# Kernel optimization log

Measured on AMD Instinct MI355X. Metric: run time of the kernel, lower is better.

The kernel has to match this reference:

```python
import jax, jax.numpy as jnp
import numpy as np
import math

DIM = 32
CODEBOOK_SIZE = 16384
LOG_N = int(math.log(CODEBOOK_SIZE, 2))  # 14
LOGVAR_MIN, LOGVAR_MAX = -30.0, 20.0
TOL = 0.5
BETA = 1.0
LAM = 1.0
LAM_MIN = 1.0
LAM_MAX = 1.0
HALF_LOG_2PI = 0.5 * math.log(2.0 * math.pi)


def setup_inputs() -> dict:
    key = jax.random.key(0)
    k1, k2, k3 = jax.random.split(key, 3)
    z = jax.random.normal(k1, (4, 512, 512), dtype=jnp.float32)
    noise = jax.random.normal(k2, (2048, 256), dtype=jnp.float32)
    # prior_samples buffer: standard-normal codebook [K, DIM]
    codebook = jax.random.normal(k3, (CODEBOOK_SIZE, DIM), dtype=jnp.float32)
    return {"z": z, "noise": noise, "codebook": codebook}


def _forward(z, noise, codebook):
    z_shape = z.shape
    zf = z.reshape(-1, z_shape[-1])                       # [N_tok, 2*DIM*cb]
    cb_num = zf.shape[-1] // (2 * DIM)                    # codebook_num
    mu, logvar = jnp.split(zf, 2, axis=-1)                # each [N_tok, DIM*cb]
    logvar = jnp.clip(logvar, LOGVAR_MIN, LOGVAR_MAX)
    std = jnp.exp(0.5 * logvar)
    var = jnp.exp(logvar)

    # ---- quant_gaussian ----
    zhat_g = mu + noise * std                             # reparam sample
    kl2 = 1.4426 * 0.5 * (mu * mu + var - 1.0 - logvar)
    kl2 = kl2.reshape(-1, DIM, cb_num).sum(axis=1)        # [N_tok, cb]
    ge = (kl2 > LOG_N + TOL).astype(kl2.dtype) * LAM_MAX
    eq = ((kl2 <= LOG_N + TOL) & (kl2 >= LOG_N - TOL)).astype(kl2.dtype)
    le = (kl2 < LOG_N - TOL).astype(kl2.dtype) * LAM_MIN
    kl_loss = jnp.mean(ge * kl2 + eq * kl2 + le * kl2) * LAM

    # ---- quant_vq (Gaussian log-likelihood-ratio codebook search) ----
    # rows: (token, codebook_num) pairs, each with a DIM-dim Gaussian
    mu_r = mu.reshape(-1, DIM, cb_num).transpose(0, 2, 1).reshape(-1, DIM)    # [N, DIM]
    std_r = std.reshape(-1, DIM, cb_num).transpose(0, 2, 1).reshape(-1, DIM)  # [N, DIM]
    inv_var = 1.0 / (std_r * std_r)                                           # [N, DIM]

    c = codebook                                          # [K, DIM]
    c2 = c * c
    # sum_d Normal(mu, std).log_prob(c) expanded into GEMMs over DIM:
    #   -sum log std - DIM/2*log(2pi) - 0.5*(c^2 - 2 c mu + mu^2) / var
    termA = -jnp.sum(jnp.log(std_r), axis=-1) - DIM * HALF_LOG_2PI            # [N]
    quad = 0.5 * (jnp.einsum('nd,kd->nk', inv_var, c2)
                  - 2.0 * jnp.einsum('nd,kd->nk', mu_r * inv_var, c)
                  + jnp.sum(mu_r * mu_r * inv_var, axis=-1, keepdims=True))   # [N, K]
    prior_lp = jnp.sum(-0.5 * c2 - HALF_LOG_2PI, axis=-1)                     # [K]
    perturbed = termA[:, None] - quad - BETA * prior_lp[None, :]              # [N, K]

    indices = jnp.argmax(perturbed, axis=1)               # [N]
    zhat_v = c[indices]                                   # [N, DIM]

    zhat_v = zhat_v.reshape(-1, cb_num, DIM).transpose(0, 2, 1).reshape(-1, cb_num * DIM)
    zhat_v = zhat_v.reshape(*z_shape[:-1], -1)            # [..., DIM*cb]
    zhat_g = zhat_g.reshape(*z_shape[:-1], -1)
    indices = indices.reshape(*z_shape[:-1], cb_num)

    # straight-through estimator (use_ste=True); vq branch is no_grad in torch
    zhat = zhat_g - jax.lax.stop_gradient(zhat_g) + jax.lax.stop_gradient(zhat_v)
    return zhat, kl_loss, indices


def reference(z, noise, codebook):
    return _forward(z, noise, codebook)
```

## Files before the change

kernel.cpp:

```cpp
#include <hip/hip_runtime.h>
#include <math.h>


typedef _Float16 half8 __attribute__((ext_vector_type(8)));
typedef float f32x4 __attribute__((ext_vector_type(4)));

#define DIM 32
#define NROWS 16384
#define NSPLIT 16
#define SPLITK 1024
#define NCOL 256

#define WS_M1   0
#define WS_KL   256
#define WS_PQ   4096
#define WS_AH   (WS_PQ + 4194304)
#define WS_BH   (WS_AH + 2097152)
#define WS_W1   (WS_BH + 2097152)

__global__ __launch_bounds__(256) void prep_kernel(const float* __restrict__ cb,
                                                   const float* __restrict__ z,
                                                   _Float16* __restrict__ Bh,
                                                   float* __restrict__ M1,
                                                   float* __restrict__ PQ,
                                                   _Float16* __restrict__ Ah,
                                                   double* __restrict__ klsum) {
  const int w = threadIdx.x >> 6, l = threadIdx.x & 63;
  const int sub = l >> 5, d = l & 31;
  if (blockIdx.x < 512) {
    __shared__ float lm[8][DIM];
    float m = 0.0f;
#pragma unroll
    for (int i = 0; i < 4; ++i) {
      const int k = blockIdx.x * 32 + i * 8 + w * 2 + sub;
      const float c = cb[k * DIM + d];
      const int key = k & 7;
      const int sc = (d >> 3) ^ key;
      const int sq = (4 + (d >> 3)) ^ key;
      Bh[(size_t)k * 64 + sc * 8 + (d & 7)] = (_Float16)c;
      Bh[(size_t)k * 64 + sq * 8 + (d & 7)] = (_Float16)(c * c);
      m = fmaxf(m, fabsf(c));
    }
    lm[threadIdx.x >> 5][d] = m;
    __syncthreads();
    if (threadIdx.x < DIM) {
      float x = lm[0][threadIdx.x];
#pragma unroll
      for (int i = 1; i < 8; ++i) x = fmaxf(x, lm[i][threadIdx.x]);
      atomicMax((unsigned*)&M1[threadIdx.x], __float_as_uint(x));
    }
  } else {
    const int blk = blockIdx.x - 512;
    double kacc = 0.0;
#pragma unroll 1
    for (int i = 0; i < 4; ++i) {
      const int row = blk * 32 + i * 8 + w * 2 + sub;
      const int t = row >> 3, c = row & 7;
      const float mu = z[t * 512 + d * 8 + c];
      float lv = z[t * 512 + 256 + d * 8 + c];
      lv = fminf(fmaxf(lv, -30.0f), 20.0f);
      const float stdv = expf(0.5f * lv);
      const float iv = 1.0f / (stdv * stdv);
      const float p = mu * iv;
      const float q = 0.5f * (1.0f - iv);
      PQ[(size_t)row * 64 + d] = p;
      PQ[(size_t)row * 64 + 32 + d] = q;
      Ah[(size_t)row * 64 + d] = (_Float16)p;
      Ah[(size_t)row * 64 + 32 + d] = (_Float16)q;
      kacc += (double)(mu * mu + stdv * stdv - 1.0f - lv);
    }
#pragma unroll
    for (int off = 32; off > 0; off >>= 1) kacc += __shfl_down(kacc, off);
    __shared__ double wsum[4];
    if (l == 0) wsum[w] = kacc;
    __syncthreads();
    if (threadIdx.x == 0)
      atomicAdd(klsum, (wsum[0] + wsum[1]) + (wsum[2] + wsum[3]));
  }
}

__device__ __forceinline__ void gload_lds16(const _Float16* g, _Float16* l) {
  __builtin_amdgcn_global_load_lds(
      (__attribute__((address_space(1))) void*)(g),
      (__attribute__((address_space(3))) void*)(l), 16, 0, 0);
}

__global__ __launch_bounds__(256, 4) void filter_kernel(const _Float16* __restrict__ Ah,
                                                        const _Float16* __restrict__ Bh,
                                                        float* __restrict__ W1) {
  __shared__ _Float16 sB[2][8192];
  const int tid = threadIdx.x;
  const int lane = tid & 63;
  const int wave = tid >> 6;
  const int split = blockIdx.y;
  const int rowbase = blockIdx.x * 256 + wave * 64;
  const int c16 = lane & 15, quad = lane >> 4;

  const _Float16* gB = Bh + (size_t)split * SPLITK * 64;

#pragma unroll
  for (int j = 0; j < 4; ++j)
    gload_lds16(gB + j * 2048 + tid * 8, &sB[0][j * 2048 + tid * 8]);

  half8 uh0[4], uh1[4];
#pragma unroll
  for (int rt = 0; rt < 4; ++rt) {
    const size_t abase = (size_t)(rowbase + rt * 16 + c16) * 64 + quad * 8;
    uh0[rt] = *(const half8*)(Ah + abase);
    uh1[rt] = *(const half8*)(Ah + abase + 32);
  }

  float a1[4][4];
#pragma unroll
  for (int rt = 0; rt < 4; ++rt)
#pragma unroll
    for (int r = 0; r < 4; ++r) a1[rt][r] = -INFINITY;

  const f32x4 fzero = {0.f, 0.f, 0.f, 0.f};
  const int key = c16 & 7;
  const int rs0h = c16 * 64 + (quad ^ key) * 8;
  const int rs1h = c16 * 64 + ((quad + 4) ^ key) * 8;

  __syncthreads();

#pragma unroll 1
  for (int ch = 0; ch < 8; ++ch) {
    if (ch < 7) {
      const _Float16* src = gB + (size_t)(ch + 1) * 8192;
      _Float16* dst = &sB[(ch + 1) & 1][0];
#pragma unroll
      for (int j = 0; j < 4; ++j)
        gload_lds16(src + j * 2048 + tid * 8, dst + j * 2048 + tid * 8);
    }
    const _Float16* buf = &sB[ch & 1][0];
#pragma unroll 1
    for (int tp = 0; tp < 4; ++tp) {
      const _Float16* b0 = buf + (2 * tp) * 1024;
      const _Float16* b1 = b0 + 1024;
      const half8 x0 = *(const half8*)(b0 + rs0h);
      const half8 x1 = *(const half8*)(b0 + rs1h);
      const half8 y0 = *(const half8*)(b1 + rs0h);
      const half8 y1 = *(const half8*)(b1 + rs1h);
#pragma unroll
      for (int rt = 0; rt < 4; ++rt) {
        f32x4 h0 = __builtin_amdgcn_mfma_f32_16x16x32_f16(uh0[rt], x0, fzero, 0, 0, 0);
        h0 = __builtin_amdgcn_mfma_f32_16x16x32_f16(uh1[rt], x1, h0, 0, 0, 0);
        f32x4 h1 = __builtin_amdgcn_mfma_f32_16x16x32_f16(uh0[rt], y0, fzero, 0, 0, 0);
        h1 = __builtin_amdgcn_mfma_f32_16x16x32_f16(uh1[rt], y1, h1, 0, 0, 0);
#pragma unroll
        for (int r = 0; r < 4; ++r)
          a1[rt][r] = fmaxf(fmaxf(h0[r], h1[r]), a1[rt][r]);
      }
    }
    __syncthreads();
  }

#pragma unroll
  for (int rt = 0; rt < 4; ++rt)
#pragma unroll
    for (int r = 0; r < 4; ++r) {
      const int row_r = rowbase + rt * 16 + quad * 4 + r;
      W1[((size_t)split * NROWS + row_r) * 16 + c16] = a1[rt][r];
    }
}

__device__ __forceinline__ float exact_score(const float4* __restrict__ cb4,
                                             const float4* __restrict__ spq,
                                             int k) {
  float s0 = 0.0f, s1 = 0.0f, s2 = 0.0f, s3 = 0.0f;
#pragma unroll
  for (int m = 0; m < 8; ++m) {
    const float4 cv = cb4[k * 8 + m];
    const float4 pv = spq[m];
    const float4 qv = spq[8 + m];
    s0 = fmaf(cv.x, fmaf(qv.x, cv.x, pv.x), s0);
    s1 = fmaf(cv.y, fmaf(qv.y, cv.y, pv.y), s1);
    s2 = fmaf(cv.z, fmaf(qv.z, cv.z, pv.z), s2);
    s3 = fmaf(cv.w, fmaf(qv.w, cv.w, pv.w), s3);
  }
  return (s0 + s1) + (s2 + s3);
}

__global__ __launch_bounds__(256, 4) void merge_kernel(const float* __restrict__ PQ,
                                                       const float* __restrict__ cb,
                                                       const float* __restrict__ W1,
                                                       const float* __restrict__ M1,
                                                       const double* __restrict__ klsum,
                                                       float* __restrict__ out0,
                                                       float* __restrict__ out1,
                                                       float* __restrict__ out2) {
  __shared__ float4 spq_s[4][16];
  const int lane = threadIdx.x & 63;
  const int wave = threadIdx.x >> 6;
  const int row = blockIdx.x * 4 + wave;

  if (lane < 16)
    spq_s[wave][lane] = ((const float4*)(PQ + (size_t)row * 64))[lane];
  __syncthreads();
  const float4* spq = spq_s[wave];
  const float4* __restrict__ cb4 = (const float4*)cb;

  float s = 0.0f;
  if (lane < DIM) {
    const float m1 = M1[lane];
    const float pd = ((const float*)spq)[lane];
    const float qd = ((const float*)spq)[32 + lane];
    s = fabsf(pd) * m1 + fabsf(qd) * m1 * m1;
  }
#pragma unroll
  for (int off = 1; off < 32; off <<= 1) s += __shfl_xor(s, off);
  const float Sn = __shfl(s, 0);

  float w[4];
#pragma unroll
  for (int i = 0; i < 4; ++i)
    w[i] = W1[((size_t)(i * 4 + (lane >> 4)) * NROWS + row) * 16 + (lane & 15)];
  float As = fmaxf(fmaxf(w[0], w[1]), fmaxf(w[2], w[3]));
#pragma unroll
  for (int off = 1; off < 64; off <<= 1) As = fmaxf(As, __shfl_xor(As, off));
  const float Btot = 1.05e-3f * Sn + 2e-5f * (fabsf(As) + 1.0f) + 1e-3f;

  int done_col = -1;
#pragma unroll
  for (int i = 0; i < 4; ++i) {
    if (done_col < 0) {
      const unsigned long long m = __ballot(w[i] == As);
      if (m) done_col = i * 64 + __builtin_ctzll(m);
    }
  }
  const int k0 = (done_col >> 4) * SPLITK + lane * 16 + (done_col & 15);
  float best = exact_score(cb4, spq, k0);
  int bk = k0;
#pragma unroll
  for (int off = 1; off < 64; off <<= 1) {
    const float ov = __shfl_xor(best, off);
    const int ok = __shfl_xor(bk, off);
    if (ov > best || (ov == best && ok < bk)) { best = ov; bk = ok; }
  }
  const float Estar = best;

#pragma unroll 1
  for (int i = 0; i < 4; ++i) {
    unsigned long long m = __ballot(w[i] + Btot >= Estar);
    if ((done_col >> 6) == i) m &= ~(1ull << (done_col & 63));
    while (m) {
      const int e = __builtin_ctzll(m);
      m &= m - 1;
      const int col = i * 64 + e;
      const int k = (col >> 4) * SPLITK + lane * 16 + (col & 15);
      const float sc = exact_score(cb4, spq, k);
      if (sc > best || (sc == best && k < bk)) { best = sc; bk = k; }
    }
  }
#pragma unroll
  for (int off = 1; off < 64; off <<= 1) {
    const float ov = __shfl_xor(best, off);
    const int ok = __shfl_xor(bk, off);
    if (ov > best || (ov == best && ok < bk)) { best = ov; bk = ok; }
  }
  if (lane == 0) out2[row] = (float)bk;
  const int tt = row >> 3, cc = row & 7;
  if (lane < DIM) out0[tt * 256 + lane * 8 + cc] = cb[bk * DIM + lane];
  if (blockIdx.x == 0 && threadIdx.x == 0)
    out1[0] = (float)(klsum[0] * (1.4426 * 0.5) / (double)NROWS);
}

extern "C" void kernel_launch(void* const* d_in, const int* in_sizes, int n_in,
                              void* d_out, int out_size, void* d_ws, size_t ws_size,
                              hipStream_t stream) {
  const float* z  = (const float*)d_in[0];
  const float* cb = (const float*)d_in[2];

  char* ws = (char*)d_ws;
  float*      M1 = (float*)(ws + WS_M1);
  double* klsum  = (double*)(ws + WS_KL);
  float*      PQ = (float*)(ws + WS_PQ);
  _Float16*   Ah = (_Float16*)(ws + WS_AH);
  _Float16*   Bh = (_Float16*)(ws + WS_BH);
  float*      W1 = (float*)(ws + WS_W1);

  float* out0 = (float*)d_out;
  float* out1 = out0 + 524288;
  float* out2 = out1 + 1;

  (void)hipMemsetAsync(ws, 0, 4096, stream);
  prep_kernel<<<1024, 256, 0, stream>>>(cb, z, Bh, M1, PQ, Ah, klsum);
  dim3 fgrid(64, NSPLIT);
  filter_kernel<<<fgrid, 256, 0, stream>>>(Ah, Bh, W1);
  merge_kernel<<<NROWS / 4, 256, 0, stream>>>(PQ, cb, W1, M1, klsum,
                                              out0, out1, out2);
}
```

Measured before the change: 134.8 us.

## Keep codebook tiles in registers and stream rows through MFMA filter

The filter kernel is restructured so each block holds a 128-entry codebook slice in registers and streams 512 query rows per wave from global memory. This drops the LDS double-buffering and the block barriers. Partial maxima now cover contiguous groups of 64 codebook entries, reduced across lanes with shuffles, and W1 is stored column-major so the merge kernel can read it coalesced. The merge kernel also swizzles its block order. In exchange there are more cross-lane shuffles and scattered per-row stores, and codebook grouping changes, which alters which candidates get rescored.

```diff
diff --git a/kernel.cpp b/kernel.cpp
--- a/kernel.cpp
+++ b/kernel.cpp
@@ -7,8 +7,11 @@
 
 #define DIM 32
 #define NROWS 16384
-#define NSPLIT 16
-#define SPLITK 1024
+#define KSIZE 16384
+#define KBLK 128
+#define NKB (KSIZE / KBLK)
+#define RGRP 8
+#define NRT 32
 #define NCOL 256
 
 #define WS_M1   0
@@ -34,11 +37,8 @@
     for (int i = 0; i < 4; ++i) {
       const int k = blockIdx.x * 32 + i * 8 + w * 2 + sub;
       const float c = cb[k * DIM + d];
-      const int key = k & 7;
-      const int sc = (d >> 3) ^ key;
-      const int sq = (4 + (d >> 3)) ^ key;
-      Bh[(size_t)k * 64 + sc * 8 + (d & 7)] = (_Float16)c;
-      Bh[(size_t)k * 64 + sq * 8 + (d & 7)] = (_Float16)(c * c);
+      Bh[(size_t)k * 64 + d] = (_Float16)c;
+      Bh[(size_t)k * 64 + 32 + d] = (_Float16)(c * c);
       m = fmaxf(m, fabsf(c));
     }
     lm[threadIdx.x >> 5][d] = m;
@@ -79,89 +79,73 @@
   }
 }
 
-__device__ __forceinline__ void gload_lds16(const _Float16* g, _Float16* l) {
-  __builtin_amdgcn_global_load_lds(
-      (__attribute__((address_space(1))) void*)(g),
-      (__attribute__((address_space(3))) void*)(l), 16, 0, 0);
-}
-
 __global__ __launch_bounds__(256, 4) void filter_kernel(const _Float16* __restrict__ Ah,
                                                         const _Float16* __restrict__ Bh,
                                                         float* __restrict__ W1) {
-  __shared__ _Float16 sB[2][8192];
-  const int tid = threadIdx.x;
-  const int lane = tid & 63;
-  const int wave = tid >> 6;
-  const int split = blockIdx.y;
-  const int rowbase = blockIdx.x * 256 + wave * 64;
+  const int lane = threadIdx.x & 63;
+  const int wave = threadIdx.x >> 6;
   const int c16 = lane & 15, quad = lane >> 4;
-
-  const _Float16* gB = Bh + (size_t)split * SPLITK * 64;
-
-#pragma unroll
-  for (int j = 0; j < 4; ++j)
-    gload_lds16(gB + j * 2048 + tid * 8, &sB[0][j * 2048 + tid * 8]);
-
-  half8 uh0[4], uh1[4];
-#pragma unroll
-  for (int rt = 0; rt < 4; ++rt) {
-    const size_t abase = (size_t)(rowbase + rt * 16 + c16) * 64 + quad * 8;
-    uh0[rt] = *(const half8*)(Ah + abase);
-    uh1[rt] = *(const half8*)(Ah + abase + 32);
-  }
-
-  float a1[4][4];
-#pragma unroll
-  for (int rt = 0; rt < 4; ++rt)
-#pragma unroll
-    for (int r = 0; r < 4; ++r) a1[rt][r] = -INFINITY;
+  const int kbase = blockIdx.y * KBLK;
+  const int col0 = blockIdx.y * 2;
+  const int rowbase0 = blockIdx.x * 2048 + wave * 512;
+
+  half8 bx0[8], bx1[8];
+#pragma unroll
+  for (int t = 0; t < 8; ++t) {
+    const size_t bb = (size_t)(kbase + t * 16 + c16) * 64 + quad * 8;
+    bx0[t] = *(const half8*)(Bh + bb);
+    bx1[t] = *(const half8*)(Bh + bb + 32);
+  }
 
   const f32x4 fzero = {0.f, 0.f, 0.f, 0.f};
-  const int key = c16 & 7;
-  const int rs0h = c16 * 64 + (quad ^ key) * 8;
-  const int rs1h = c16 * 64 + ((quad + 4) ^ key) * 8;
-
-  __syncthreads();
+  const size_t astep = 16 * 64;
+  size_t acur = (size_t)(rowbase0 + c16) * 64 + quad * 8;
+  half8 u0 = *(const half8*)(Ah + acur);
+  half8 u1 = *(const half8*)(Ah + acur + 32);
 
 #pragma unroll 1
-  for (int ch = 0; ch < 8; ++ch) {
-    if (ch < 7) {
-      const _Float16* src = gB + (size_t)(ch + 1) * 8192;
-      _Float16* dst = &sB[(ch + 1) & 1][0];
-#pragma unroll
-      for (int j = 0; j < 4; ++j)
-        gload_lds16(src + j * 2048 + tid * 8, dst + j * 2048 + tid * 8);
-    }
-    const _Float16* buf = &sB[ch & 1][0];
-#pragma unroll 1
-    for (int tp = 0; tp < 4; ++tp) {
-      const _Float16* b0 = buf + (2 * tp) * 1024;
-      const _Float16* b1 = b0 + 1024;
-      const half8 x0 = *(const half8*)(b0 + rs0h);
-      const half8 x1 = *(const half8*)(b0 + rs1h);
-      const half8 y0 = *(const half8*)(b1 + rs0h);
-      const half8 y1 = *(const half8*)(b1 + rs1h);
-#pragma unroll
-      for (int rt = 0; rt < 4; ++rt) {
-        f32x4 h0 = __builtin_amdgcn_mfma_f32_16x16x32_f16(uh0[rt], x0, fzero, 0, 0, 0);
-        h0 = __builtin_amdgcn_mfma_f32_16x16x32_f16(uh1[rt], x1, h0, 0, 0, 0);
-        f32x4 h1 = __builtin_amdgcn_mfma_f32_16x16x32_f16(uh0[rt], y0, fzero, 0, 0, 0);
-        h1 = __builtin_amdgcn_mfma_f32_16x16x32_f16(uh1[rt], y1, h1, 0, 0, 0);
-#pragma unroll
-        for (int r = 0; r < 4; ++r)
-          a1[rt][r] = fmaxf(fmaxf(h0[r], h1[r]), a1[rt][r]);
+  for (int rt = 0; rt < NRT; ++rt) {
+    half8 n0, n1;
+    if (rt + 1 < NRT) {
+      n0 = *(const half8*)(Ah + acur + astep);
+      n1 = *(const half8*)(Ah + acur + astep + 32);
+    }
+    f32x4 m0 = __builtin_amdgcn_mfma_f32_16x16x32_f16(u0, bx0[0], fzero, 0, 0, 0);
+    m0 = __builtin_amdgcn_mfma_f32_16x16x32_f16(u1, bx1[0], m0, 0, 0, 0);
+#pragma unroll
+    for (int t = 1; t < 4; ++t) {
+      f32x4 h = __builtin_amdgcn_mfma_f32_16x16x32_f16(u0, bx0[t], fzero, 0, 0, 0);
+      h = __builtin_amdgcn_mfma_f32_16x16x32_f16(u1, bx1[t], h, 0, 0, 0);
+#pragma unroll
+      for (int r = 0; r < 4; ++r) m0[r] = fmaxf(m0[r], h[r]);
+    }
+    f32x4 m1 = __builtin_amdgcn_mfma_f32_16x16x32_f16(u0, bx0[4], fzero, 0, 0, 0);
+    m1 = __builtin_amdgcn_mfma_f32_16x16x32_f16(u1, bx1[4], m1, 0, 0, 0);
+#pragma unroll
+    for (int t = 5; t < 8; ++t) {
+      f32x4 h = __builtin_amdgcn_mfma_f32_16x16x32_f16(u0, bx0[t], fzero, 0, 0, 0);
+      h = __builtin_amdgcn_mfma_f32_16x16x32_f16(u1, bx1[t], h, 0, 0, 0);
+#pragma unroll
+      for (int r = 0; r < 4; ++r) m1[r] = fmaxf(m1[r], h[r]);
+    }
+#pragma unroll
+    for (int mask = 1; mask <= 8; mask <<= 1) {
+#pragma unroll
+      for (int r = 0; r < 4; ++r) {
+        m0[r] = fmaxf(m0[r], __shfl_xor(m0[r], mask));
+        m1[r] = fmaxf(m1[r], __shfl_xor(m1[r], mask));
       }
     }
-    __syncthreads();
-  }
-
-#pragma unroll
-  for (int rt = 0; rt < 4; ++rt)
-#pragma unroll
-    for (int r = 0; r < 4; ++r) {
-      const int row_r = rowbase + rt * 16 + quad * 4 + r;
-      W1[((size_t)split * NROWS + row_r) * 16 + c16] = a1[rt][r];
-    }
+    if (c16 == 0) {
+      const int rowo = rowbase0 + rt * 16 + quad * 4;
+#pragma unroll
+      for (int r = 0; r < 4; ++r) {
+        W1[(size_t)col0 * NROWS + rowo + r] = m0[r];
+        W1[(size_t)(col0 + 1) * NROWS + rowo + r] = m1[r];
+      }
+    }
+    u0 = n0; u1 = n1; acur += astep;
+  }
 }
 
 __device__ __forceinline__ float exact_score(const float4* __restrict__ cb4,
@@ -192,7 +176,8 @@
   __shared__ float4 spq_s[4][16];
   const int lane = threadIdx.x & 63;
   const int wave = threadIdx.x >> 6;
-  const int row = blockIdx.x * 4 + wave;
+  const int bswz = (blockIdx.x & 7) * 512 + (blockIdx.x >> 3);
+  const int row = bswz * 4 + wave;
 
   if (lane < 16)
     spq_s[wave][lane] = ((const float4*)(PQ + (size_t)row * 64))[lane];
@@ -214,7 +199,7 @@
   float w[4];
 #pragma unroll
   for (int i = 0; i < 4; ++i)
-    w[i] = W1[((size_t)(i * 4 + (lane >> 4)) * NROWS + row) * 16 + (lane & 15)];
+    w[i] = W1[(size_t)(i * 64 + lane) * NROWS + row];
   float As = fmaxf(fmaxf(w[0], w[1]), fmaxf(w[2], w[3]));
 #pragma unroll
   for (int off = 1; off < 64; off <<= 1) As = fmaxf(As, __shfl_xor(As, off));
@@ -228,7 +213,7 @@
       if (m) done_col = i * 64 + __builtin_ctzll(m);
     }
   }
-  const int k0 = (done_col >> 4) * SPLITK + lane * 16 + (done_col & 15);
+  const int k0 = done_col * 64 + lane;
   float best = exact_score(cb4, spq, k0);
   int bk = k0;
 #pragma unroll
@@ -247,7 +232,7 @@
       const int e = __builtin_ctzll(m);
       m &= m - 1;
       const int col = i * 64 + e;
-      const int k = (col >> 4) * SPLITK + lane * 16 + (col & 15);
+      const int k = col * 64 + lane;
       const float sc = exact_score(cb4, spq, k);
       if (sc > best || (sc == best && k < bk)) { best = sc; bk = k; }
     }
@@ -285,7 +270,7 @@
 
   (void)hipMemsetAsync(ws, 0, 4096, stream);
   prep_kernel<<<1024, 256, 0, stream>>>(cb, z, Bh, M1, PQ, Ah, klsum);
-  dim3 fgrid(64, NSPLIT);
+  dim3 fgrid(RGRP, NKB);
   filter_kernel<<<fgrid, 256, 0, stream>>>(Ah, Bh, W1);
   merge_kernel<<<NROWS / 4, 256, 0, stream>>>(PQ, cb, W1, M1, klsum,
                                               out0, out1, out2);
```

Result: slower. 176.2 us (+30.7%).

## Stream codebook tiles from global into registers instead of staging through LDS

Applied to the files above, without the earlier changes.

The filter kernel stops double-buffering codebook tiles in shared memory with global_load_lds. Each wave now loads its 16-code B fragment straight from global (L2) into registers, prefetching the next tile one step ahead. To keep the reuse ratio, each wave covers 128 rows (8 row tiles) and the grid halves. The codebook swizzle in prep is dropped since LDS bank conflicts no longer matter. In exchange every wave fetches B separately (more L2 traffic), uses more registers (launch bounds 2), and has fewer blocks to hide latency with.

```diff
diff --git a/kernel.cpp b/kernel.cpp
--- a/kernel.cpp
+++ b/kernel.cpp
@@ -7,6 +7,7 @@
 
 #define DIM 32
 #define NROWS 16384
+#define KSIZE 16384
 #define NSPLIT 16
 #define SPLITK 1024
 #define NCOL 256
@@ -34,11 +35,8 @@
     for (int i = 0; i < 4; ++i) {
       const int k = blockIdx.x * 32 + i * 8 + w * 2 + sub;
       const float c = cb[k * DIM + d];
-      const int key = k & 7;
-      const int sc = (d >> 3) ^ key;
-      const int sq = (4 + (d >> 3)) ^ key;
-      Bh[(size_t)k * 64 + sc * 8 + (d & 7)] = (_Float16)c;
-      Bh[(size_t)k * 64 + sq * 8 + (d & 7)] = (_Float16)(c * c);
+      Bh[(size_t)k * 64 + d] = (_Float16)c;
+      Bh[(size_t)k * 64 + 32 + d] = (_Float16)(c * c);
       m = fmaxf(m, fabsf(c));
     }
     lm[threadIdx.x >> 5][d] = m;
@@ -79,84 +77,55 @@
   }
 }
 
-__device__ __forceinline__ void gload_lds16(const _Float16* g, _Float16* l) {
-  __builtin_amdgcn_global_load_lds(
-      (__attribute__((address_space(1))) void*)(g),
-      (__attribute__((address_space(3))) void*)(l), 16, 0, 0);
-}
-
-__global__ __launch_bounds__(256, 4) void filter_kernel(const _Float16* __restrict__ Ah,
+__global__ __launch_bounds__(256, 2) void filter_kernel(const _Float16* __restrict__ Ah,
                                                         const _Float16* __restrict__ Bh,
                                                         float* __restrict__ W1) {
-  __shared__ _Float16 sB[2][8192];
-  const int tid = threadIdx.x;
-  const int lane = tid & 63;
-  const int wave = tid >> 6;
+  const int lane = threadIdx.x & 63;
+  const int wave = threadIdx.x >> 6;
+  const int c16 = lane & 15, quad = lane >> 4;
   const int split = blockIdx.y;
-  const int rowbase = blockIdx.x * 256 + wave * 64;
-  const int c16 = lane & 15, quad = lane >> 4;
-
+  const int rowbase = blockIdx.x * 512 + wave * 128;
+
+  half8 u0[8], u1[8];
+#pragma unroll
+  for (int rt = 0; rt < 8; ++rt) {
+    const size_t ab = (size_t)(rowbase + rt * 16 + c16) * 64 + quad * 8;
+    u0[rt] = *(const half8*)(Ah + ab);
+    u1[rt] = *(const half8*)(Ah + ab + 32);
+  }
+
+  float a1[8][4];
+#pragma unroll
+  for (int rt = 0; rt < 8; ++rt)
+#pragma unroll
+    for (int r = 0; r < 4; ++r) a1[rt][r] = -INFINITY;
+
+  const f32x4 fzero = {0.f, 0.f, 0.f, 0.f};
   const _Float16* gB = Bh + (size_t)split * SPLITK * 64;
 
-#pragma unroll
-  for (int j = 0; j < 4; ++j)
-    gload_lds16(gB + j * 2048 + tid * 8, &sB[0][j * 2048 + tid * 8]);
-
-  half8 uh0[4], uh1[4];
-#pragma unroll
-  for (int rt = 0; rt < 4; ++rt) {
-    const size_t abase = (size_t)(rowbase + rt * 16 + c16) * 64 + quad * 8;
-    uh0[rt] = *(const half8*)(Ah + abase);
-    uh1[rt] = *(const half8*)(Ah + abase + 32);
-  }
-
-  float a1[4][4];
-#pragma unroll
-  for (int rt = 0; rt < 4; ++rt)
-#pragma unroll
-    for (int r = 0; r < 4; ++r) a1[rt][r] = -INFINITY;
-
-  const f32x4 fzero = {0.f, 0.f, 0.f, 0.f};
-  const int key = c16 & 7;
-  const int rs0h = c16 * 64 + (quad ^ key) * 8;
-  const int rs1h = c16 * 64 + ((quad + 4) ^ key) * 8;
-
-  __syncthreads();
+  half8 b0 = *(const half8*)(gB + c16 * 64 + quad * 8);
+  half8 b1 = *(const half8*)(gB + c16 * 64 + quad * 8 + 32);
 
 #pragma unroll 1
-  for (int ch = 0; ch < 8; ++ch) {
-    if (ch < 7) {
-      const _Float16* src = gB + (size_t)(ch + 1) * 8192;
-      _Float16* dst = &sB[(ch + 1) & 1][0];
-#pragma unroll
-      for (int j = 0; j < 4; ++j)
-        gload_lds16(src + j * 2048 + tid * 8, dst + j * 2048 + tid * 8);
-    }
-    const _Float16* buf = &sB[ch & 1][0];
-#pragma unroll 1
-    for (int tp = 0; tp < 4; ++tp) {
-      const _Float16* b0 = buf + (2 * tp) * 1024;
-      const _Float16* b1 = b0 + 1024;
-      const half8 x0 = *(const half8*)(b0 + rs0h);
-      const half8 x1 = *(const half8*)(b0 + rs1h);
-      const half8 y0 = *(const half8*)(b1 + rs0h);
-      const half8 y1 = *(const half8*)(b1 + rs1h);
-#pragma unroll
-      for (int rt = 0; rt < 4; ++rt) {
-        f32x4 h0 = __builtin_amdgcn_mfma_f32_16x16x32_f16(uh0[rt], x0, fzero, 0, 0, 0);
-        h0 = __builtin_amdgcn_mfma_f32_16x16x32_f16(uh1[rt], x1, h0, 0, 0, 0);
-        f32x4 h1 = __builtin_amdgcn_mfma_f32_16x16x32_f16(uh0[rt], y0, fzero, 0, 0, 0);
-        h1 = __builtin_amdgcn_mfma_f32_16x16x32_f16(uh1[rt], y1, h1, 0, 0, 0);
-#pragma unroll
-        for (int r = 0; r < 4; ++r)
-          a1[rt][r] = fmaxf(fmaxf(h0[r], h1[r]), a1[rt][r]);
-      }
-    }
-    __syncthreads();
-  }
-
-#pragma unroll
-  for (int rt = 0; rt < 4; ++rt)
+  for (int t = 0; t < 64; ++t) {
+    half8 n0, n1;
+    if (t < 63) {
+      const _Float16* nb = gB + (size_t)((t + 1) * 16 + c16) * 64 + quad * 8;
+      n0 = *(const half8*)(nb);
+      n1 = *(const half8*)(nb + 32);
+    }
+#pragma unroll
+    for (int rt = 0; rt < 8; ++rt) {
+      f32x4 h = __builtin_amdgcn_mfma_f32_16x16x32_f16(u0[rt], b0, fzero, 0, 0, 0);
+      h = __builtin_amdgcn_mfma_f32_16x16x32_f16(u1[rt], b1, h, 0, 0, 0);
+#pragma unroll
+      for (int r = 0; r < 4; ++r) a1[rt][r] = fmaxf(a1[rt][r], h[r]);
+    }
+    b0 = n0; b1 = n1;
+  }
+
+#pragma unroll
+  for (int rt = 0; rt < 8; ++rt)
 #pragma unroll
     for (int r = 0; r < 4; ++r) {
       const int row_r = rowbase + rt * 16 + quad * 4 + r;
@@ -285,7 +254,7 @@
 
   (void)hipMemsetAsync(ws, 0, 4096, stream);
   prep_kernel<<<1024, 256, 0, stream>>>(cb, z, Bh, M1, PQ, Ah, klsum);
-  dim3 fgrid(64, NSPLIT);
+  dim3 fgrid(32, NSPLIT);
   filter_kernel<<<fgrid, 256, 0, stream>>>(Ah, Bh, W1);
   merge_kernel<<<NROWS / 4, 256, 0, stream>>>(PQ, cb, W1, M1, klsum,
                                               out0, out1, out2);
```

Measured after the change: 159.1 us. +18.0%, slower.
